# Kernel tuning notes

Measured on AMD Instinct MI355X. Metric: run time of the kernel, lower is better.

Reference implementation:

```python
import jax, jax.numpy as jnp
import numpy as np

B, D, C, K = 8192, 2048, 4096, 1000  # batch, input_dim, num_centers, num_classes


def setup_inputs() -> dict:
    key = jax.random.key(0)
    k0, k1, k2 = jax.random.split(key, 3)
    x = jax.random.normal(k0, (B, D), dtype=jnp.float32)
    centers = jax.random.normal(k1, (C, D), dtype=jnp.float32)
    beta = jnp.ones((C,), dtype=jnp.float32)
    W = jax.random.normal(k2, (K, C), dtype=jnp.float32) * 0.02  # fc.weight
    b = jnp.zeros((K,), dtype=jnp.float32)  # fc.bias
    return {"x": x, "centers": centers, "beta": beta, "W": W, "b": b}


def reference(x, centers, beta, W, b):
    # Pairwise Euclidean distance via the Gram trick (same math as
    # torch.norm(x[:,None,:] - centers, dim=2), without the (B,C,D) intermediate).
    x2 = jnp.sum(x * x, axis=-1, keepdims=True)          # (B, 1)
    c2 = jnp.sum(centers * centers, axis=-1)             # (C,)
    sq = x2 + c2[None, :] - 2.0 * (x @ centers.T)        # (B, C) squared distances
    dist = jnp.sqrt(jnp.maximum(sq, 0.0))
    act = jnp.exp(-beta[None, :] * dist)                 # RBF activations
    act = act / jnp.sum(act, axis=1, keepdims=True)      # normalize over centers
    return act @ W.T + b                                 # linear head (B, K)
```

## Files before the change

kernel.cpp:

```cpp
#include <hip/hip_runtime.h>


#define BB 8192
#define DD 2048
#define CC 4096
#define KK 1000
#define KP 1024

typedef unsigned short u16;
typedef __bf16 bf16x8 __attribute__((ext_vector_type(8)));
typedef float f32x4 __attribute__((ext_vector_type(4)));

typedef const void __attribute__((address_space(1)))* gvp_t;
typedef void __attribute__((address_space(3)))* lvp_t;

__device__ __forceinline__ u16 f2bf(float f) {
  union { float f; unsigned u; } v; v.f = f;
  return (u16)((v.u + 0x7fffu + ((v.u >> 16) & 1u)) >> 16);
}

__global__ void prep_norm_cast(const float* __restrict__ x, const float* __restrict__ cen,
                               u16* __restrict__ xb, u16* __restrict__ cb,
                               float* __restrict__ x2, float* __restrict__ c2) {
  int row = blockIdx.x;
  const float* src;
  u16* dst;
  float* nrm;
  if (row < BB) {
    src = x + (size_t)row * DD; dst = xb + (size_t)row * DD; nrm = x2 + row;
  } else {
    int r = row - BB;
    src = cen + (size_t)r * DD; dst = cb + (size_t)r * DD; nrm = c2 + r;
  }
  int t = threadIdx.x;
  float s = 0.f;
#pragma unroll
  for (int m = 0; m < 2; ++m) {
    int idx = t + 256 * m;
    float4 v = reinterpret_cast<const float4*>(src)[idx];
    s += v.x * v.x + v.y * v.y + v.z * v.z + v.w * v.w;
    reinterpret_cast<ushort4*>(dst)[idx] =
        make_ushort4(f2bf(v.x), f2bf(v.y), f2bf(v.z), f2bf(v.w));
  }
#pragma unroll
  for (int off = 1; off < 64; off <<= 1) s += __shfl_xor(s, off);
  __shared__ float red[4];
  if ((t & 63) == 0) red[t >> 6] = s;
  __syncthreads();
  if (t == 0) *nrm = red[0] + red[1] + red[2] + red[3];
}

__global__ void prep_wcast(const float* __restrict__ W, u16* __restrict__ wb) {
  int row = blockIdx.x;
  int t = threadIdx.x;
  ushort4* dst = reinterpret_cast<ushort4*>(wb + (size_t)row * CC);
  if (row < KK) {
    const float4* src = reinterpret_cast<const float4*>(W + (size_t)row * CC);
#pragma unroll
    for (int m = 0; m < 4; ++m) {
      float4 v = src[t + 256 * m];
      dst[t + 256 * m] = make_ushort4(f2bf(v.x), f2bf(v.y), f2bf(v.z), f2bf(v.w));
    }
  } else {
#pragma unroll
    for (int m = 0; m < 4; ++m) dst[t + 256 * m] = make_ushort4(0, 0, 0, 0);
  }
}

__global__ void gemm1_rbf(const u16* __restrict__ Abf, const u16* __restrict__ Bbf,
                          const float* __restrict__ x2, const float* __restrict__ c2,
                          const float* __restrict__ beta, u16* __restrict__ Ebf,
                          float* __restrict__ rowsum) {
  constexpr int Kd = DD;
  __shared__ __align__(16) char smem[32768];

  const int t = threadIdx.x;
  const int lane = t & 63;
  const int wave = t >> 6;
  const int wr = wave >> 1, wc = wave & 1;
  const int l15 = lane & 15, quad = lane >> 4;

  const int rowBase = blockIdx.y * 128;
  const int colBase = blockIdx.x * 128;

  f32x4 acc[4][4];
  f32x4 z4 = {0.f, 0.f, 0.f, 0.f};
#pragma unroll
  for (int i = 0; i < 4; ++i)
#pragma unroll
    for (int j = 0; j < 4; ++j) acc[i][j] = z4;

  const int sr = t >> 3;
  const int sc = t & 7;

  for (int kc = 0; kc < Kd; kc += 64) {
#pragma unroll
    for (int it = 0; it < 4; ++it) {
      int r = sr + 32 * it;
      int sw = (sc ^ (r & 7)) * 8;
      const u16* ga = Abf + (size_t)(rowBase + r) * Kd + kc + sw;
      const u16* gb = Bbf + (size_t)(colBase + r) * Kd + kc + sw;
      char* la = smem + it * 4096 + t * 16;
      char* lb = smem + 16384 + it * 4096 + t * 16;
      __builtin_amdgcn_global_load_lds((gvp_t)ga, (lvp_t)la, 16, 0, 0);
      __builtin_amdgcn_global_load_lds((gvp_t)gb, (lvp_t)lb, 16, 0, 0);
    }
    __syncthreads();
#pragma unroll
    for (int ks = 0; ks < 2; ++ks) {
      bf16x8 af[4], bfr[4];
#pragma unroll
      for (int i = 0; i < 4; ++i) {
        int r = wr * 64 + i * 16 + l15;
        int slot = (ks * 4 + quad) ^ (r & 7);
        af[i] = *(const bf16x8*)(smem + r * 128 + slot * 16);
      }
#pragma unroll
      for (int j = 0; j < 4; ++j) {
        int r = wc * 64 + j * 16 + l15;
        int slot = (ks * 4 + quad) ^ (r & 7);
        bfr[j] = *(const bf16x8*)(smem + 16384 + r * 128 + slot * 16);
      }
#pragma unroll
      for (int j = 0; j < 4; ++j)
#pragma unroll
        for (int i = 0; i < 4; ++i)
          acc[i][j] = __builtin_amdgcn_mfma_f32_16x16x32_bf16(af[i], bfr[j], acc[i][j], 0, 0, 0);
    }
    __syncthreads();
  }

  const int rbase = rowBase + wr * 64;
  const int cbase = colBase + wc * 64;
  float x2r[4][4];
#pragma unroll
  for (int i = 0; i < 4; ++i)
#pragma unroll
    for (int r = 0; r < 4; ++r) x2r[i][r] = x2[rbase + i * 16 + quad * 4 + r];

  float rs[4][4];
#pragma unroll
  for (int i = 0; i < 4; ++i)
#pragma unroll
    for (int r = 0; r < 4; ++r) rs[i][r] = 0.f;

#pragma unroll
  for (int j = 0; j < 4; ++j) {
    int cg = cbase + j * 16 + l15;
    float c2v = c2[cg];
    float bet = beta[cg];
#pragma unroll
    for (int i = 0; i < 4; ++i) {
      int rg0 = rbase + i * 16 + quad * 4;
#pragma unroll
      for (int r = 0; r < 4; ++r) {
        float d = acc[i][j][r];
        float sq = fmaxf(x2r[i][r] + c2v - 2.0f * d, 0.0f);
        float e = expf(-bet * sqrtf(sq));
        Ebf[(size_t)(rg0 + r) * CC + cg] = f2bf(e);
        rs[i][r] += e;
      }
    }
  }
#pragma unroll
  for (int i = 0; i < 4; ++i)
#pragma unroll
    for (int r = 0; r < 4; ++r) {
      float v = rs[i][r];
      v += __shfl_xor(v, 1);
      v += __shfl_xor(v, 2);
      v += __shfl_xor(v, 4);
      v += __shfl_xor(v, 8);
      if (l15 == 0) atomicAdd(&rowsum[rbase + i * 16 + quad * 4 + r], v);
    }
}

__global__ void gemm2_out(const u16* __restrict__ Ebf, const u16* __restrict__ Wbf,
                          const float* __restrict__ rowsum, const float* __restrict__ bias,
                          float* __restrict__ out) {
  constexpr int Kd = CC;
  __shared__ __align__(16) char smem[32768];

  const int t = threadIdx.x;
  const int lane = t & 63;
  const int wave = t >> 6;
  const int wr = wave >> 1, wc = wave & 1;
  const int l15 = lane & 15, quad = lane >> 4;

  const int rowBase = blockIdx.y * 128;
  const int colBase = blockIdx.x * 128;

  f32x4 acc[4][4];
  f32x4 z4 = {0.f, 0.f, 0.f, 0.f};
#pragma unroll
  for (int i = 0; i < 4; ++i)
#pragma unroll
    for (int j = 0; j < 4; ++j) acc[i][j] = z4;

  const int sr = t >> 3;
  const int sc = t & 7;

  for (int kc = 0; kc < Kd; kc += 64) {
#pragma unroll
    for (int it = 0; it < 4; ++it) {
      int r = sr + 32 * it;
      int sw = (sc ^ (r & 7)) * 8;
      const u16* ga = Ebf + (size_t)(rowBase + r) * Kd + kc + sw;
      const u16* gb = Wbf + (size_t)(colBase + r) * Kd + kc + sw;
      char* la = smem + it * 4096 + t * 16;
      char* lb = smem + 16384 + it * 4096 + t * 16;
      __builtin_amdgcn_global_load_lds((gvp_t)ga, (lvp_t)la, 16, 0, 0);
      __builtin_amdgcn_global_load_lds((gvp_t)gb, (lvp_t)lb, 16, 0, 0);
    }
    __syncthreads();
#pragma unroll
    for (int ks = 0; ks < 2; ++ks) {
      bf16x8 af[4], bfr[4];
#pragma unroll
      for (int i = 0; i < 4; ++i) {
        int r = wr * 64 + i * 16 + l15;
        int slot = (ks * 4 + quad) ^ (r & 7);
        af[i] = *(const bf16x8*)(smem + r * 128 + slot * 16);
      }
#pragma unroll
      for (int j = 0; j < 4; ++j) {
        int r = wc * 64 + j * 16 + l15;
        int slot = (ks * 4 + quad) ^ (r & 7);
        bfr[j] = *(const bf16x8*)(smem + 16384 + r * 128 + slot * 16);
      }
#pragma unroll
      for (int j = 0; j < 4; ++j)
#pragma unroll
        for (int i = 0; i < 4; ++i)
          acc[i][j] = __builtin_amdgcn_mfma_f32_16x16x32_bf16(af[i], bfr[j], acc[i][j], 0, 0, 0);
    }
    __syncthreads();
  }

  const int rbase = rowBase + wr * 64;
  const int cbase = colBase + wc * 64;
  float inv[4][4];
#pragma unroll
  for (int i = 0; i < 4; ++i)
#pragma unroll
    for (int r = 0; r < 4; ++r) inv[i][r] = 1.0f / rowsum[rbase + i * 16 + quad * 4 + r];

#pragma unroll
  for (int j = 0; j < 4; ++j) {
    int cg = cbase + j * 16 + l15;
    if (cg < KK) {
      float bv = bias[cg];
#pragma unroll
      for (int i = 0; i < 4; ++i) {
        int rg0 = rbase + i * 16 + quad * 4;
#pragma unroll
        for (int r = 0; r < 4; ++r)
          out[(size_t)(rg0 + r) * KK + cg] = acc[i][j][r] * inv[i][r] + bv;
      }
    }
  }
}

#define OFF_XB 0u
#define OFF_CB 33554432u
#define OFF_WB 50331648u
#define OFF_EB 58720256u
#define OFF_X2 125829120u
#define OFF_C2 125861888u
#define OFF_RS 125878272u

extern "C" void kernel_launch(void* const* d_in, const int* in_sizes, int n_in,
                              void* d_out, int out_size, void* d_ws, size_t ws_size,
                              hipStream_t stream) {
  const float* x = (const float*)d_in[0];
  const float* cen = (const float*)d_in[1];
  const float* beta = (const float*)d_in[2];
  const float* W = (const float*)d_in[3];
  const float* bias = (const float*)d_in[4];
  float* out = (float*)d_out;
  char* ws = (char*)d_ws;

  u16* xb = (u16*)(ws + OFF_XB);
  u16* cb = (u16*)(ws + OFF_CB);
  u16* wb = (u16*)(ws + OFF_WB);
  u16* eb = (u16*)(ws + OFF_EB);
  float* x2 = (float*)(ws + OFF_X2);
  float* c2 = (float*)(ws + OFF_C2);
  float* rowsum = (float*)(ws + OFF_RS);

  hipMemsetAsync(rowsum, 0, BB * sizeof(float), stream);
  prep_norm_cast<<<BB + CC, 256, 0, stream>>>(x, cen, xb, cb, x2, c2);
  prep_wcast<<<KP, 256, 0, stream>>>(W, wb);
  gemm1_rbf<<<dim3(CC / 128, BB / 128), 256, 0, stream>>>(xb, cb, x2, c2, beta, eb, rowsum);
  gemm2_out<<<dim3(KP / 128, BB / 128), 256, 0, stream>>>(eb, wb, rowsum, bias, out);
}
```

Measured before the change: 410.1 us.

## Switch GEMMs to 32x32x16 MFMA, enlarge GEMM1 tile, compute rowsum separately

Both GEMMs now use the 32x32x16 bf16 MFMA instead of 16x16x32, which lowers LDS fragment reads per FLOP. GEMM1 grows its tile to 256x128 with 48KB LDS and launch bounds, uses fast __expf and sqrt intrinsics, and drops the atomic rowsum accumulation. A new rowsum kernel instead re-reads the bf16 activations, which adds 64MB of traffic and a launch but removes the memset and the atomics. The row sum is now taken over bf16-rounded values, so precision changes slightly.

```diff
diff --git a/kernel.cpp b/kernel.cpp
--- a/kernel.cpp
+++ b/kernel.cpp
@@ -9,7 +9,7 @@
 
 typedef unsigned short u16;
 typedef __bf16 bf16x8 __attribute__((ext_vector_type(8)));
-typedef float f32x4 __attribute__((ext_vector_type(4)));
+typedef float f32x16 __attribute__((ext_vector_type(16)));
 
 typedef const void __attribute__((address_space(1)))* gvp_t;
 typedef void __attribute__((address_space(3)))* lvp_t;
@@ -17,6 +17,10 @@
 __device__ __forceinline__ u16 f2bf(float f) {
   union { float f; unsigned u; } v; v.f = f;
   return (u16)((v.u + 0x7fffu + ((v.u >> 16) & 1u)) >> 16);
+}
+__device__ __forceinline__ float bf2f(u16 h) {
+  union { unsigned u; float f; } v; v.u = ((unsigned)h) << 16;
+  return v.f;
 }
 
 __global__ void prep_norm_cast(const float* __restrict__ x, const float* __restrict__ cen,
@@ -67,117 +71,123 @@
   }
 }
 
-__global__ void gemm1_rbf(const u16* __restrict__ Abf, const u16* __restrict__ Bbf,
-                          const float* __restrict__ x2, const float* __restrict__ c2,
-                          const float* __restrict__ beta, u16* __restrict__ Ebf,
-                          float* __restrict__ rowsum) {
+__global__ __launch_bounds__(256, 2)
+void gemm1_rbf(const u16* __restrict__ Abf, const u16* __restrict__ Bbf,
+               const float* __restrict__ x2, const float* __restrict__ c2,
+               const float* __restrict__ beta, u16* __restrict__ Ebf) {
   constexpr int Kd = DD;
-  __shared__ __align__(16) char smem[32768];
+  __shared__ __align__(16) char smem[49152];
 
   const int t = threadIdx.x;
   const int lane = t & 63;
   const int wave = t >> 6;
   const int wr = wave >> 1, wc = wave & 1;
-  const int l15 = lane & 15, quad = lane >> 4;
-
-  const int rowBase = blockIdx.y * 128;
+  const int l31 = lane & 31, khalf = lane >> 5;
+
+  const int rowBase = blockIdx.y * 256;
   const int colBase = blockIdx.x * 128;
 
-  f32x4 acc[4][4];
-  f32x4 z4 = {0.f, 0.f, 0.f, 0.f};
+  f32x16 acc[4][2];
 #pragma unroll
   for (int i = 0; i < 4; ++i)
 #pragma unroll
-    for (int j = 0; j < 4; ++j) acc[i][j] = z4;
+    for (int j = 0; j < 2; ++j) acc[i][j] = 0.f;
 
   const int sr = t >> 3;
-  const int sc = t & 7;
+  const int srcChunkOff = ((t & 7) ^ ((t >> 3) & 7)) * 8;
+  const u16* gA0 = Abf + (size_t)(rowBase + sr) * Kd + srcChunkOff;
+  const u16* gB0 = Bbf + (size_t)(colBase + sr) * Kd + srcChunkOff;
+
+  const int xorv = l31 & 7;
 
   for (int kc = 0; kc < Kd; kc += 64) {
 #pragma unroll
+    for (int it = 0; it < 8; ++it) {
+      const u16* ga = gA0 + (size_t)(32 * it) * Kd + kc;
+      __builtin_amdgcn_global_load_lds((gvp_t)ga, (lvp_t)(smem + it * 4096 + t * 16), 16, 0, 0);
+    }
+#pragma unroll
     for (int it = 0; it < 4; ++it) {
-      int r = sr + 32 * it;
-      int sw = (sc ^ (r & 7)) * 8;
-      const u16* ga = Abf + (size_t)(rowBase + r) * Kd + kc + sw;
-      const u16* gb = Bbf + (size_t)(colBase + r) * Kd + kc + sw;
-      char* la = smem + it * 4096 + t * 16;
-      char* lb = smem + 16384 + it * 4096 + t * 16;
-      __builtin_amdgcn_global_load_lds((gvp_t)ga, (lvp_t)la, 16, 0, 0);
-      __builtin_amdgcn_global_load_lds((gvp_t)gb, (lvp_t)lb, 16, 0, 0);
+      const u16* gb = gB0 + (size_t)(32 * it) * Kd + kc;
+      __builtin_amdgcn_global_load_lds((gvp_t)gb, (lvp_t)(smem + 32768 + it * 4096 + t * 16), 16, 0, 0);
     }
     __syncthreads();
 #pragma unroll
-    for (int ks = 0; ks < 2; ++ks) {
-      bf16x8 af[4], bfr[4];
+    for (int ks = 0; ks < 4; ++ks) {
+      const int slot = ((ks * 2 + khalf) ^ xorv) * 16;
+      bf16x8 af[4], bfr[2];
 #pragma unroll
       for (int i = 0; i < 4; ++i) {
-        int r = wr * 64 + i * 16 + l15;
-        int slot = (ks * 4 + quad) ^ (r & 7);
-        af[i] = *(const bf16x8*)(smem + r * 128 + slot * 16);
-      }
-#pragma unroll
-      for (int j = 0; j < 4; ++j) {
-        int r = wc * 64 + j * 16 + l15;
-        int slot = (ks * 4 + quad) ^ (r & 7);
-        bfr[j] = *(const bf16x8*)(smem + 16384 + r * 128 + slot * 16);
-      }
-#pragma unroll
-      for (int j = 0; j < 4; ++j)
+        int r = wr * 128 + i * 32 + l31;
+        af[i] = *(const bf16x8*)(smem + r * 128 + slot);
+      }
+#pragma unroll
+      for (int j = 0; j < 2; ++j) {
+        int r = wc * 64 + j * 32 + l31;
+        bfr[j] = *(const bf16x8*)(smem + 32768 + r * 128 + slot);
+      }
+#pragma unroll
+      for (int j = 0; j < 2; ++j)
 #pragma unroll
         for (int i = 0; i < 4; ++i)
-          acc[i][j] = __builtin_amdgcn_mfma_f32_16x16x32_bf16(af[i], bfr[j], acc[i][j], 0, 0, 0);
+          acc[i][j] = __builtin_amdgcn_mfma_f32_32x32x16_bf16(af[i], bfr[j], acc[i][j], 0, 0, 0);
     }
     __syncthreads();
   }
 
-  const int rbase = rowBase + wr * 64;
+  const int rbase = rowBase + wr * 128 + 4 * khalf;
   const int cbase = colBase + wc * 64;
-  float x2r[4][4];
-#pragma unroll
-  for (int i = 0; i < 4; ++i)
-#pragma unroll
-    for (int r = 0; r < 4; ++r) x2r[i][r] = x2[rbase + i * 16 + quad * 4 + r];
-
-  float rs[4][4];
-#pragma unroll
-  for (int i = 0; i < 4; ++i)
-#pragma unroll
-    for (int r = 0; r < 4; ++r) rs[i][r] = 0.f;
-
-#pragma unroll
-  for (int j = 0; j < 4; ++j) {
-    int cg = cbase + j * 16 + l15;
-    float c2v = c2[cg];
-    float bet = beta[cg];
-#pragma unroll
-    for (int i = 0; i < 4; ++i) {
-      int rg0 = rbase + i * 16 + quad * 4;
-#pragma unroll
-      for (int r = 0; r < 4; ++r) {
-        float d = acc[i][j][r];
-        float sq = fmaxf(x2r[i][r] + c2v - 2.0f * d, 0.0f);
-        float e = expf(-bet * sqrtf(sq));
-        Ebf[(size_t)(rg0 + r) * CC + cg] = f2bf(e);
-        rs[i][r] += e;
-      }
-    }
-  }
-#pragma unroll
-  for (int i = 0; i < 4; ++i)
-#pragma unroll
-    for (int r = 0; r < 4; ++r) {
-      float v = rs[i][r];
-      v += __shfl_xor(v, 1);
-      v += __shfl_xor(v, 2);
-      v += __shfl_xor(v, 4);
-      v += __shfl_xor(v, 8);
-      if (l15 == 0) atomicAdd(&rowsum[rbase + i * 16 + quad * 4 + r], v);
-    }
-}
-
-__global__ void gemm2_out(const u16* __restrict__ Ebf, const u16* __restrict__ Wbf,
-                          const float* __restrict__ rowsum, const float* __restrict__ bias,
-                          float* __restrict__ out) {
+  float c2v[2], bet[2];
+  int gcol[2];
+#pragma unroll
+  for (int j = 0; j < 2; ++j) {
+    gcol[j] = cbase + j * 32 + l31;
+    c2v[j] = c2[gcol[j]];
+    bet[j] = beta[gcol[j]];
+  }
+#pragma unroll
+  for (int i = 0; i < 4; ++i) {
+#pragma unroll
+    for (int reg = 0; reg < 16; ++reg) {
+      int grow = rbase + i * 32 + (reg & 3) + 8 * (reg >> 2);
+      float x2v = x2[grow];
+#pragma unroll
+      for (int j = 0; j < 2; ++j) {
+        float d = acc[i][j][reg];
+        float sq = fmaxf(x2v + c2v[j] - 2.0f * d, 0.0f);
+        float e = __expf(-bet[j] * __builtin_amdgcn_sqrtf(sq));
+        Ebf[(size_t)grow * CC + gcol[j]] = f2bf(e);
+      }
+    }
+  }
+}
+
+__global__ void rowsum_k(const u16* __restrict__ Ebf, float* __restrict__ rowsum) {
+  const int lane = threadIdx.x & 63;
+  const int row = blockIdx.x * 4 + (threadIdx.x >> 6);
+  const uint4* p = reinterpret_cast<const uint4*>(Ebf + (size_t)row * CC);
+  float s = 0.f;
+#pragma unroll
+  for (int it = 0; it < 8; ++it) {
+    uint4 v = p[lane + 64 * it];
+    unsigned w[4] = {v.x, v.y, v.z, v.w};
+#pragma unroll
+    for (int q = 0; q < 4; ++q) {
+      union { unsigned u; float f; } lo, hi;
+      lo.u = w[q] << 16;
+      hi.u = w[q] & 0xffff0000u;
+      s += lo.f + hi.f;
+    }
+  }
+#pragma unroll
+  for (int off = 1; off < 64; off <<= 1) s += __shfl_xor(s, off);
+  if (lane == 0) rowsum[row] = s;
+}
+
+__global__ __launch_bounds__(256, 3)
+void gemm2_out(const u16* __restrict__ Ebf, const u16* __restrict__ Wbf,
+               const float* __restrict__ rowsum, const float* __restrict__ bias,
+               float* __restrict__ out) {
   constexpr int Kd = CC;
   __shared__ __align__(16) char smem[32768];
 
@@ -185,77 +195,77 @@
   const int lane = t & 63;
   const int wave = t >> 6;
   const int wr = wave >> 1, wc = wave & 1;
-  const int l15 = lane & 15, quad = lane >> 4;
+  const int l31 = lane & 31, khalf = lane >> 5;
 
   const int rowBase = blockIdx.y * 128;
   const int colBase = blockIdx.x * 128;
 
-  f32x4 acc[4][4];
-  f32x4 z4 = {0.f, 0.f, 0.f, 0.f};
-#pragma unroll
-  for (int i = 0; i < 4; ++i)
-#pragma unroll
-    for (int j = 0; j < 4; ++j) acc[i][j] = z4;
+  f32x16 acc[2][2];
+#pragma unroll
+  for (int i = 0; i < 2; ++i)
+#pragma unroll
+    for (int j = 0; j < 2; ++j) acc[i][j] = 0.f;
 
   const int sr = t >> 3;
-  const int sc = t & 7;
+  const int srcChunkOff = ((t & 7) ^ ((t >> 3) & 7)) * 8;
+  const u16* gA0 = Ebf + (size_t)(rowBase + sr) * Kd + srcChunkOff;
+  const u16* gB0 = Wbf + (size_t)(colBase + sr) * Kd + srcChunkOff;
+  const int xorv = l31 & 7;
 
   for (int kc = 0; kc < Kd; kc += 64) {
 #pragma unroll
     for (int it = 0; it < 4; ++it) {
-      int r = sr + 32 * it;
-      int sw = (sc ^ (r & 7)) * 8;
-      const u16* ga = Ebf + (size_t)(rowBase + r) * Kd + kc + sw;
-      const u16* gb = Wbf + (size_t)(colBase + r) * Kd + kc + sw;
-      char* la = smem + it * 4096 + t * 16;
-      char* lb = smem + 16384 + it * 4096 + t * 16;
-      __builtin_amdgcn_global_load_lds((gvp_t)ga, (lvp_t)la, 16, 0, 0);
-      __builtin_amdgcn_global_load_lds((gvp_t)gb, (lvp_t)lb, 16, 0, 0);
+      const u16* ga = gA0 + (size_t)(32 * it) * Kd + kc;
+      __builtin_amdgcn_global_load_lds((gvp_t)ga, (lvp_t)(smem + it * 4096 + t * 16), 16, 0, 0);
+    }
+#pragma unroll
+    for (int it = 0; it < 4; ++it) {
+      const u16* gb = gB0 + (size_t)(32 * it) * Kd + kc;
+      __builtin_amdgcn_global_load_lds((gvp_t)gb, (lvp_t)(smem + 16384 + it * 4096 + t * 16), 16, 0, 0);
     }
     __syncthreads();
 #pragma unroll
-    for (int ks = 0; ks < 2; ++ks) {
-      bf16x8 af[4], bfr[4];
-#pragma unroll
-      for (int i = 0; i < 4; ++i) {
-        int r = wr * 64 + i * 16 + l15;
-        int slot = (ks * 4 + quad) ^ (r & 7);
-        af[i] = *(const bf16x8*)(smem + r * 128 + slot * 16);
-      }
-#pragma unroll
-      for (int j = 0; j < 4; ++j) {
-        int r = wc * 64 + j * 16 + l15;
-        int slot = (ks * 4 + quad) ^ (r & 7);
-        bfr[j] = *(const bf16x8*)(smem + 16384 + r * 128 + slot * 16);
-      }
-#pragma unroll
-      for (int j = 0; j < 4; ++j)
-#pragma unroll
-        for (int i = 0; i < 4; ++i)
-          acc[i][j] = __builtin_amdgcn_mfma_f32_16x16x32_bf16(af[i], bfr[j], acc[i][j], 0, 0, 0);
+    for (int ks = 0; ks < 4; ++ks) {
+      const int slot = ((ks * 2 + khalf) ^ xorv) * 16;
+      bf16x8 af[2], bfr[2];
+#pragma unroll
+      for (int i = 0; i < 2; ++i) {
+        int r = wr * 64 + i * 32 + l31;
+        af[i] = *(const bf16x8*)(smem + r * 128 + slot);
+      }
+#pragma unroll
+      for (int j = 0; j < 2; ++j) {
+        int r = wc * 64 + j * 32 + l31;
+        bfr[j] = *(const bf16x8*)(smem + 16384 + r * 128 + slot);
+      }
+#pragma unroll
+      for (int j = 0; j < 2; ++j)
+#pragma unroll
+        for (int i = 0; i < 2; ++i)
+          acc[i][j] = __builtin_amdgcn_mfma_f32_32x32x16_bf16(af[i], bfr[j], acc[i][j], 0, 0, 0);
     }
     __syncthreads();
   }
 
-  const int rbase = rowBase + wr * 64;
+  const int rbase = rowBase + wr * 64 + 4 * khalf;
   const int cbase = colBase + wc * 64;
-  float inv[4][4];
-#pragma unroll
-  for (int i = 0; i < 4; ++i)
-#pragma unroll
-    for (int r = 0; r < 4; ++r) inv[i][r] = 1.0f / rowsum[rbase + i * 16 + quad * 4 + r];
-
-#pragma unroll
-  for (int j = 0; j < 4; ++j) {
-    int cg = cbase + j * 16 + l15;
-    if (cg < KK) {
-      float bv = bias[cg];
-#pragma unroll
-      for (int i = 0; i < 4; ++i) {
-        int rg0 = rbase + i * 16 + quad * 4;
-#pragma unroll
-        for (int r = 0; r < 4; ++r)
-          out[(size_t)(rg0 + r) * KK + cg] = acc[i][j][r] * inv[i][r] + bv;
+  int gcol[2];
+  float bv[2];
+#pragma unroll
+  for (int j = 0; j < 2; ++j) {
+    gcol[j] = cbase + j * 32 + l31;
+    bv[j] = (gcol[j] < KK) ? bias[gcol[j]] : 0.f;
+  }
+#pragma unroll
+  for (int i = 0; i < 2; ++i) {
+#pragma unroll
+    for (int reg = 0; reg < 16; ++reg) {
+      int grow = rbase + i * 32 + (reg & 3) + 8 * (reg >> 2);
+      float inv = 1.0f / rowsum[grow];
+#pragma unroll
+      for (int j = 0; j < 2; ++j) {
+        if (gcol[j] < KK)
+          out[(size_t)grow * KK + gcol[j]] = acc[i][j][reg] * inv + bv[j];
       }
     }
   }
@@ -288,9 +298,9 @@
   float* c2 = (float*)(ws + OFF_C2);
   float* rowsum = (float*)(ws + OFF_RS);
 
-  hipMemsetAsync(rowsum, 0, BB * sizeof(float), stream);
   prep_norm_cast<<<BB + CC, 256, 0, stream>>>(x, cen, xb, cb, x2, c2);
   prep_wcast<<<KP, 256, 0, stream>>>(W, wb);
-  gemm1_rbf<<<dim3(CC / 128, BB / 128), 256, 0, stream>>>(xb, cb, x2, c2, beta, eb, rowsum);
+  gemm1_rbf<<<dim3(CC / 128, BB / 256), 256, 0, stream>>>(xb, cb, x2, c2, beta, eb);
+  rowsum_k<<<BB / 4, 256, 0, stream>>>(eb, rowsum);
   gemm2_out<<<dim3(KP / 128, BB / 128), 256, 0, stream>>>(eb, wb, rowsum, bias, out);
 }
```

New measurement: 390.2 us. -4.8%, faster.
